# Kernel optimization log

Hardware: AMD Instinct MI355X
Metric: run time of the kernel (lower is better)

## Reference

```python
import jax, jax.numpy as jnp
import numpy as np

D_IN = 768
D_SAE = 24576
BATCH = 2048
K = 64


def setup_inputs() -> dict:
    key = jax.random.key(0)
    k1, k2 = jax.random.split(key)
    x = jax.random.normal(k1, (BATCH, D_IN), dtype=jnp.float32)
    # kaiming-uniform-ish init then unit-norm rows (set_decoder_norm_to_unit_norm)
    bound = np.sqrt(6.0 / D_SAE)
    W_dec = jax.random.uniform(k2, (D_SAE, D_IN), minval=-bound, maxval=bound, dtype=jnp.float32)
    W_dec = W_dec / jnp.linalg.norm(W_dec, axis=1, keepdims=True)
    W_enc = W_dec.T  # tied at init (W_dec.t().clone())
    b_enc = jnp.zeros((D_SAE,), dtype=jnp.float32)
    b_dec = jnp.zeros((D_IN,), dtype=jnp.float32)
    return {"x": x, "W_enc": W_enc, "W_dec": W_dec, "b_enc": b_enc, "b_dec": b_dec, "k": K}


def topk_activation(pre, k):
    # torch.topk -> relu(values) -> scatter into zeros
    vals, idx = jax.lax.top_k(pre, k)            # [B, k]
    vals = jax.nn.relu(vals)
    rows = jnp.arange(pre.shape[0])[:, None]     # [B, 1]
    return jnp.zeros_like(pre).at[rows, idx].set(vals)


def reference(x, W_enc, W_dec, b_enc, b_dec, k):
    # normalize=False -> preprocess is identity
    xc = x - b_dec
    latents_pre_act = xc @ W_enc + b_enc         # [B, d_sae]
    latents = topk_activation(latents_pre_act, k)
    recons = latents @ W_dec + b_dec             # [B, d_in]
    mse_loss = jnp.sum((recons - x) ** 2)        # F.mse_loss(reduction='sum')
    return mse_loss
```

## Files before the change

kernel.cpp:

```cpp
#include <hip/hip_runtime.h>
#include <hip/hip_bf16.h>
#include <stdint.h>
#include <string.h>

#define D_IN 768
#define D_SAE 24576
#define BATCH 2048
#define TOPK 64
#define CAP 1024
#define CAPB 120
#define KEY_LIM 0xC000u

typedef _Float16 f16x8 __attribute__((ext_vector_type(8)));
typedef _Float16 f16x4 __attribute__((ext_vector_type(4)));
typedef float floatx4 __attribute__((ext_vector_type(4)));

#define AS1 __attribute__((address_space(1)))
#define AS3 __attribute__((address_space(3)))

__device__ __forceinline__ void load_lds16(const void* g, void* l) {
    __builtin_amdgcn_global_load_lds((AS1 void*)(g), (AS3 void*)(l), 16, 0, 0);
}

__global__ __launch_bounds__(256) void prep_x_kernel(const float* __restrict__ x,
                                                     const float* __restrict__ b_dec,
                                                     _Float16* __restrict__ xch,
                                                     int* __restrict__ cnt,
                                                     float* __restrict__ out) {
    int t = blockIdx.x * 256 + threadIdx.x;
    if (t == 0) out[0] = 0.0f;
    if (t < BATCH) cnt[t] = 0;
    int i = t * 4;
    if (i >= BATCH * D_IN) return;
    int c = i % D_IN;
    float4 xv = *(const float4*)(x + i);
    float4 bv = *(const float4*)(b_dec + c);
    f16x4 h;
    h[0] = (_Float16)(xv.x - bv.x);
    h[1] = (_Float16)(xv.y - bv.y);
    h[2] = (_Float16)(xv.z - bv.z);
    h[3] = (_Float16)(xv.w - bv.w);
    *(f16x4*)(xch + i) = h;
}

__global__ __launch_bounds__(256) void transpose_kernel(const float* __restrict__ W,
                                                        _Float16* __restrict__ WT) {
    __shared__ _Float16 tile[32][33];
    int n0 = blockIdx.x * 32;
    int k0 = blockIdx.y * 32;
    int tx = threadIdx.x & 31, ty = threadIdx.x >> 5;
#pragma unroll
    for (int r = 0; r < 4; ++r) {
        int k = k0 + ty + r * 8;
        tile[ty + r * 8][tx] = (_Float16)W[(size_t)k * D_SAE + n0 + tx];
    }
    __syncthreads();
#pragma unroll
    for (int r = 0; r < 4; ++r) {
        int n = n0 + ty + r * 8;
        WT[(size_t)n * D_IN + k0 + tx] = tile[tx][ty + r * 8];
    }
}


#define TE 16384

#define BAR() do { __builtin_amdgcn_sched_barrier(0);            \
                   asm volatile("s_barrier" ::: "memory");       \
                   __builtin_amdgcn_sched_barrier(0); } while (0)
#define WLG() do { asm volatile("s_waitcnt lgkmcnt(0)" ::: "memory"); \
                   __builtin_amdgcn_sched_barrier(0); } while (0)

__global__ __launch_bounds__(512, 2) void gemm_kernel(const _Float16* __restrict__ A,
                                                      const _Float16* __restrict__ BT,
                                                      const float* __restrict__ b_enc,
                                                      int* __restrict__ cnt,
                                                      unsigned* __restrict__ cand) {
    __shared__ __align__(16) char smem[131072];
    _Float16* As = (_Float16*)smem;
    _Float16* Bs = (_Float16*)(smem + 65536);

    const int tid = threadIdx.x;
    const int lane = tid & 63;
    const int wave = tid >> 6;
    const int wm = wave >> 2;
    const int wn = wave & 3;

    const int bid = blockIdx.x;
    const int swz = (bid & 7) * 96 + (bid >> 3);
    const int m0 = (swz & 7) * 256;
    const int n0 = (swz >> 3) * 256;

    const int drow = lane >> 3;
    const int g8 = ((lane & 7) ^ drow) * 8;
    const _Float16* Ath = A + (size_t)(m0 + drow) * D_IN + g8;
    const _Float16* Bth = BT + (size_t)(n0 + drow) * D_IN + g8;
    const int arb = wave * 8;
    const int brb = ((wave >> 2) << 6) + (wave & 3) * 8;

    const int colv = lane & 15, quad = lane >> 4;
    const int sw = colv & 7;
    const int o0 = ((quad) ^ sw) * 8;
    const int o1 = ((quad + 4) ^ sw) * 8;
    const int amr = (wm * 128 + colv) * 64;
    const int bnr = (wn * 64 + colv) * 64;

    floatx4 acc[8][4];
#pragma unroll
    for (int mi = 0; mi < 8; ++mi)
#pragma unroll
        for (int ni = 0; ni < 4; ++ni)
#pragma unroll
            for (int r = 0; r < 4; ++r) acc[mi][ni][r] = 0.0f;

#define STA(CB, RB, KC) load_lds16(Ath + (size_t)(RB) * D_IN + (KC), As + (CB) * TE + (RB) * 64)
#define STB(CB, RB, KC) load_lds16(Bth + (size_t)(RB) * D_IN + (KC), Bs + (CB) * TE + (RB) * 64)

    STA(0, arb, 0);        STA(0, arb + 128, 0);
    STB(0, brb, 0);        STB(0, brb + 128, 0);
    STA(0, arb + 64, 0);   STA(0, arb + 192, 0);
    STB(0, brb + 32, 0);   STB(0, brb + 160, 0);
    STA(1, arb, 64);       STA(1, arb + 128, 64);
    STB(1, brb, 64);       STB(1, brb + 128, 64);
    STA(1, arb + 64, 64);  STA(1, arb + 192, 64);
    asm volatile("s_waitcnt vmcnt(6)" ::: "memory");
    BAR();

#define KTILE(KT, CB, S1, S2, VMN) do {                                            \
    const _Float16* Ac = As + (CB) * TE;                                           \
    const _Float16* Bc = Bs + (CB) * TE;                                           \
    const int kc1 = ((KT) + 1) * 64, kc2 = ((KT) + 2) * 64;                        \
    f16x8 alo[4][2], ahi[4][2], blo[2][2], bhi[2][2];                              \
                  \
    _Pragma("unroll") for (int mi = 0; mi < 4; ++mi) {                             \
        alo[mi][0] = *(const f16x8*)(Ac + amr + mi * 1024 + o0);                   \
        alo[mi][1] = *(const f16x8*)(Ac + amr + mi * 1024 + o1);                   \
    }                                                                              \
    _Pragma("unroll") for (int ni = 0; ni < 2; ++ni) {                             \
        blo[ni][0] = *(const f16x8*)(Bc + bnr + ni * 1024 + o0);                   \
        blo[ni][1] = *(const f16x8*)(Bc + bnr + ni * 1024 + o1);                   \
    }                                                                              \
    if (S1) { STB(1 - (CB), brb + 32, kc1); STB(1 - (CB), brb + 160, kc1); }       \
    BAR(); WLG();                                                                  \
    __builtin_amdgcn_s_setprio(1);                                                 \
    _Pragma("unroll") for (int mi = 0; mi < 4; ++mi)                               \
        _Pragma("unroll") for (int ni = 0; ni < 2; ++ni) {                         \
            acc[mi][ni] = __builtin_amdgcn_mfma_f32_16x16x32_f16(alo[mi][0], blo[ni][0], acc[mi][ni], 0, 0, 0); \
            acc[mi][ni] = __builtin_amdgcn_mfma_f32_16x16x32_f16(alo[mi][1], blo[ni][1], acc[mi][ni], 0, 0, 0); \
        }                                                                          \
    __builtin_amdgcn_s_setprio(0);                                                 \
    BAR();                                                                         \
             \
    _Pragma("unroll") for (int mi = 0; mi < 4; ++mi) {                             \
        ahi[mi][0] = *(const f16x8*)(Ac + amr + (mi + 4) * 1024 + o0);             \
        ahi[mi][1] = *(const f16x8*)(Ac + amr + (mi + 4) * 1024 + o1);             \
    }                                                                              \
    if (S2) { STA(CB, arb, kc2); STA(CB, arb + 128, kc2); }                        \
    BAR(); WLG();                                                                  \
    __builtin_amdgcn_s_setprio(1);                                                 \
    _Pragma("unroll") for (int mi = 0; mi < 4; ++mi)                               \
        _Pragma("unroll") for (int ni = 0; ni < 2; ++ni) {                         \
            acc[mi + 4][ni] = __builtin_amdgcn_mfma_f32_16x16x32_f16(ahi[mi][0], blo[ni][0], acc[mi + 4][ni], 0, 0, 0); \
            acc[mi + 4][ni] = __builtin_amdgcn_mfma_f32_16x16x32_f16(ahi[mi][1], blo[ni][1], acc[mi + 4][ni], 0, 0, 0); \
        }                                                                          \
    __builtin_amdgcn_s_setprio(0);                                                 \
    BAR();                                                                         \
             \
    _Pragma("unroll") for (int ni = 0; ni < 2; ++ni) {                             \
        bhi[ni][0] = *(const f16x8*)(Bc + bnr + (ni + 2) * 1024 + o0);             \
        bhi[ni][1] = *(const f16x8*)(Bc + bnr + (ni + 2) * 1024 + o1);             \
    }                                                                              \
    if (S2) { STB(CB, brb, kc2); STB(CB, brb + 128, kc2); }                        \
    BAR(); WLG();                                                                  \
    __builtin_amdgcn_s_setprio(1);                                                 \
    _Pragma("unroll") for (int mi = 0; mi < 4; ++mi)                               \
        _Pragma("unroll") for (int ni = 0; ni < 2; ++ni) {                         \
            acc[mi + 4][ni + 2] = __builtin_amdgcn_mfma_f32_16x16x32_f16(ahi[mi][0], bhi[ni][0], acc[mi + 4][ni + 2], 0, 0, 0); \
            acc[mi + 4][ni + 2] = __builtin_amdgcn_mfma_f32_16x16x32_f16(ahi[mi][1], bhi[ni][1], acc[mi + 4][ni + 2], 0, 0, 0); \
        }                                                                          \
    __builtin_amdgcn_s_setprio(0);                                                 \
    BAR();                                                                         \
         \
    if (S2) { STA(CB, arb + 64, kc2); STA(CB, arb + 192, kc2); }                   \
    BAR(); WLG();                                                                  \
    __builtin_amdgcn_s_setprio(1);                                                 \
    _Pragma("unroll") for (int mi = 0; mi < 4; ++mi)                               \
        _Pragma("unroll") for (int ni = 0; ni < 2; ++ni) {                         \
            acc[mi][ni + 2] = __builtin_amdgcn_mfma_f32_16x16x32_f16(alo[mi][0], bhi[ni][0], acc[mi][ni + 2], 0, 0, 0); \
            acc[mi][ni + 2] = __builtin_amdgcn_mfma_f32_16x16x32_f16(alo[mi][1], bhi[ni][1], acc[mi][ni + 2], 0, 0, 0); \
        }                                                                          \
    __builtin_amdgcn_s_setprio(0);                                                 \
    if (VMN == 6) asm volatile("s_waitcnt vmcnt(6)" ::: "memory");                 \
    else if (VMN == 0) asm volatile("s_waitcnt vmcnt(0)" ::: "memory");            \
    BAR();                                                                         \
} while (0)

    for (int kp = 0; kp < 5; ++kp) {
        const int kte = kp * 2;
        KTILE(kte, 0, 1, 1, 6);
        KTILE(kte + 1, 1, 1, 1, 6);
    }
    KTILE(10, 0, 1, 0, 0);
    KTILE(11, 1, 0, 0, -1);

#undef KTILE
#undef STA
#undef STB

    __syncthreads();
    int* lcnt      = (int*)smem;
    int* gbase     = (int*)(smem + 1024);
    unsigned* lbuf = (unsigned*)(smem + 2048);

    if (tid < 256) lcnt[tid] = 0;
    __syncthreads();

    float be[4];
#pragma unroll
    for (int ni = 0; ni < 4; ++ni) be[ni] = b_enc[n0 + wn * 64 + ni * 16 + colv];
#pragma unroll
    for (int mi = 0; mi < 8; ++mi) {
#pragma unroll
        for (int ni = 0; ni < 4; ++ni) {
            const int n_g = n0 + wn * 64 + ni * 16 + colv;
            const int lrow0 = wm * 128 + mi * 16 + quad * 4;
#pragma unroll
            for (int r = 0; r < 4; ++r) {
                _Float16 h = (_Float16)(acc[mi][ni][r] + be[ni]);
                unsigned short u;
                __builtin_memcpy(&u, &h, 2);
                unsigned key = (unsigned)(u ^ ((u & 0x8000) ? 0xFFFFu : 0x8000u));
                if (key >= KEY_LIM) {
                    int lrow = lrow0 + r;
                    int ls = atomicAdd(&lcnt[lrow], 1);
                    if (ls < CAPB) lbuf[lrow * CAPB + ls] = (key << 16) | (unsigned)n_g;
                }
            }
        }
    }
    __syncthreads();

    if (tid < 256) {
        int c = lcnt[tid];
        int g = 0;
        if (c > 0) {
            int add = (c <= CAPB) ? c : (c + CAP + 1);
            g = atomicAdd(&cnt[m0 + tid], add);
        }
        gbase[tid] = g;
    }
    __syncthreads();

    if (tid < 256) {
        int c = lcnt[tid]; if (c > CAPB) c = CAPB;
        int g = gbase[tid];
        unsigned* dst = cand + (size_t)(m0 + tid) * CAP;
        for (int j = 0; j < c; ++j) {
            int p = g + j;
            if (p < CAP) dst[p] = lbuf[tid * CAPB + j];
        }
    }
}

__global__ __launch_bounds__(256) void topk_loss_kernel(const unsigned* __restrict__ cand,
                                                        const int* __restrict__ cnt,
                                                        const _Float16* __restrict__ xch,
                                                        const _Float16* __restrict__ WT,
                                                        const float* __restrict__ b_enc,
                                                        const float* __restrict__ x,
                                                        const float* __restrict__ b_dec,
                                                        unsigned short* __restrict__ scratch,
                                                        float* __restrict__ out) {
    const int row = blockIdx.x;
    const int tid = threadIdx.x;
    const int lane = tid & 63, wv = tid >> 6;

    __shared__ unsigned cl[CAP];
    __shared__ int hist[256];
    __shared__ int wtot[4];
    __shared__ float wred[4];
    __shared__ int sh_B, sh_K, na, ne;
    __shared__ int sel_idx[TOPK];
    __shared__ float sel_val[TOPK];
    __shared__ _Float16 xs[D_IN];

    const int n_raw = cnt[row];
    const bool fast = (n_raw >= TOPK && n_raw <= CAP);
    const int N = fast ? n_raw : D_SAE;
    unsigned short* prow = scratch + (size_t)row * D_SAE;

    if (fast) {
        const unsigned* cr = cand + (size_t)row * CAP;
        for (int i = tid; i < N; i += 256) cl[i] = cr[i];
    } else {
        const _Float16* xr = xch + (size_t)row * D_IN;
        for (int i = tid; i < D_IN; i += 256) xs[i] = xr[i];
        __syncthreads();
        for (int j = tid; j < D_SAE; j += 256) {
            float s = b_enc[j];
            const _Float16* wr = WT + (size_t)j * D_IN;
            for (int k = 0; k < D_IN; ++k) s += (float)xs[k] * (float)wr[k];
            _Float16 h = (_Float16)s;
            unsigned short u;
            __builtin_memcpy(&u, &h, 2);
            prow[j] = (unsigned short)(u ^ ((u & 0x8000) ? 0xFFFFu : 0x8000u));
        }
    }
    __syncthreads();

    int K = TOPK;

    hist[tid] = 0;
    __syncthreads();
    for (int i = tid; i < N; i += 256) {
        unsigned k = fast ? (cl[i] >> 24) : ((unsigned)prow[i] >> 8);
        atomicAdd(&hist[k], 1);
    }
    __syncthreads();
    {
        int h = hist[tid], s = h;
#pragma unroll
        for (int off = 1; off < 64; off <<= 1) {
            int v = __shfl_down(s, off, 64);
            if (lane + off < 64) s += v;
        }
        if (lane == 0) wtot[wv] = s;
        __syncthreads();
        for (int w2 = wv + 1; w2 < 4; ++w2) s += wtot[w2];
        int G = s - h;
        if (G < K && s >= K) { sh_B = tid; sh_K = K - G; }
        __syncthreads();
    }
    const unsigned B = (unsigned)sh_B;
    K = sh_K;
    __syncthreads();

    hist[tid] = 0;
    __syncthreads();
    for (int i = tid; i < N; i += 256) {
        unsigned k = fast ? (cl[i] >> 16) : (unsigned)prow[i];
        if ((k >> 8) == B) atomicAdd(&hist[k & 0xFF], 1);
    }
    __syncthreads();
    {
        int h = hist[tid], s = h;
#pragma unroll
        for (int off = 1; off < 64; off <<= 1) {
            int v = __shfl_down(s, off, 64);
            if (lane + off < 64) s += v;
        }
        if (lane == 0) wtot[wv] = s;
        __syncthreads();
        for (int w2 = wv + 1; w2 < 4; ++w2) s += wtot[w2];
        int G = s - h;
        if (G < K && s >= K) { sh_B = tid; sh_K = K - G; }
        __syncthreads();
    }
    const unsigned T = (B << 8) | (unsigned)sh_B;
    const int K2 = sh_K;
    const int nGreater = TOPK - K2;

    if (tid == 0) { na = 0; ne = 0; }
    __syncthreads();
    for (int i = tid; i < N; i += 256) {
        unsigned k; int col;
        if (fast) { unsigned v = cl[i]; k = v >> 16; col = (int)(v & 0xFFFFu); }
        else      { k = (unsigned)prow[i]; col = i; }
        int slot = -1;
        if (k > T) slot = atomicAdd(&na, 1);
        else if (k == T) {
            int e = atomicAdd(&ne, 1);
            if (e < K2) slot = nGreater + e;
        }
        if (slot >= 0) {
            unsigned short u = (unsigned short)((k & 0x8000u) ? (k ^ 0x8000u) : (k ^ 0xFFFFu));
            _Float16 h;
            __builtin_memcpy(&h, &u, 2);
            sel_idx[slot] = col;
            sel_val[slot] = fmaxf((float)h, 0.0f);
        }
    }
    __syncthreads();

    const int c0 = tid, c1 = tid + 256, c2 = tid + 512;
    const float* xr = x + (size_t)row * D_IN;
    float r0 = b_dec[c0], r1 = b_dec[c1], r2 = b_dec[c2];
#pragma unroll 8
    for (int s = 0; s < TOPK; ++s) {
        float v = sel_val[s];
        const _Float16* wr = WT + (size_t)sel_idx[s] * D_IN;
        r0 += v * (float)wr[c0];
        r1 += v * (float)wr[c1];
        r2 += v * (float)wr[c2];
    }
    float d0 = r0 - xr[c0], d1 = r1 - xr[c1], d2 = r2 - xr[c2];
    float local = d0 * d0 + d1 * d1 + d2 * d2;

#pragma unroll
    for (int off = 32; off > 0; off >>= 1) local += __shfl_down(local, off, 64);
    if (lane == 0) wred[wv] = local;
    __syncthreads();
    if (tid == 0) atomicAdd(out, wred[0] + wred[1] + wred[2] + wred[3]);
}

extern "C" void kernel_launch(void* const* d_in, const int* in_sizes, int n_in,
                              void* d_out, int out_size, void* d_ws, size_t ws_size,
                              hipStream_t stream) {
    const float* x     = (const float*)d_in[0];
    const float* W_enc = (const float*)d_in[1];
    const float* W_dec = (const float*)d_in[2];
    const float* b_enc = (const float*)d_in[3];
    const float* b_dec = (const float*)d_in[4];
    float* out = (float*)d_out;

    char* ws = (char*)d_ws;
    _Float16* xch           = (_Float16*)ws;
    _Float16* WT            = (_Float16*)(ws + 3145728);
    unsigned short* scratch = (unsigned short*)(ws + 3145728 + 37748736);
    int* cnt                = (int*)(ws + 3145728 + 37748736 + 100663296);
    unsigned* cand          = (unsigned*)(ws + 3145728 + 37748736 + 100663296 + 8192);

    prep_x_kernel<<<1536, 256, 0, stream>>>(x, b_dec, xch, cnt, out);
    transpose_kernel<<<dim3(D_SAE / 32, D_IN / 32), 256, 0, stream>>>(W_enc, WT);
    gemm_kernel<<<dim3(768), 512, 0, stream>>>(xch, WT, b_enc, cnt, cand);
    topk_loss_kernel<<<BATCH, 256, 0, stream>>>(cand, cnt, xch, WT, b_enc, x, b_dec, scratch, out);
}
```

Before: 319.2 us.

## Replace global atomic candidate append with fixed per-block slots

The GEMM epilogue no longer does a global atomicAdd per row to append candidates. Each block now writes its count plus up to 30 candidates into a fixed slot indexed by (row, column block), which removes the global counter and its zeroing. The top-k kernel sums the 96 slot counts with an LDS prefix and gathers the candidates into shared memory. The fallback path now recomputes keys on the fly instead of staging them in a scratch buffer, so it does three full dot-product passes and becomes much slower. The lower per-block cap also makes that fallback more likely to trigger.

```diff
diff --git a/kernel.cpp b/kernel.cpp
--- a/kernel.cpp
+++ b/kernel.cpp
@@ -8,7 +8,9 @@
 #define BATCH 2048
 #define TOPK 64
 #define CAP 1024
-#define CAPB 120
+#define NBLK 96
+#define SLOTW 32
+#define CAPB_L 30
 #define KEY_LIM 0xC000u
 
 typedef _Float16 f16x8 __attribute__((ext_vector_type(8)));
@@ -25,11 +27,9 @@
 __global__ __launch_bounds__(256) void prep_x_kernel(const float* __restrict__ x,
                                                      const float* __restrict__ b_dec,
                                                      _Float16* __restrict__ xch,
-                                                     int* __restrict__ cnt,
                                                      float* __restrict__ out) {
     int t = blockIdx.x * 256 + threadIdx.x;
     if (t == 0) out[0] = 0.0f;
-    if (t < BATCH) cnt[t] = 0;
     int i = t * 4;
     if (i >= BATCH * D_IN) return;
     int c = i % D_IN;
@@ -74,7 +74,6 @@
 __global__ __launch_bounds__(512, 2) void gemm_kernel(const _Float16* __restrict__ A,
                                                       const _Float16* __restrict__ BT,
                                                       const float* __restrict__ b_enc,
-                                                      int* __restrict__ cnt,
                                                       unsigned* __restrict__ cand) {
     __shared__ __align__(16) char smem[131072];
     _Float16* As = (_Float16*)smem;
@@ -209,8 +208,7 @@
 
     __syncthreads();
     int* lcnt      = (int*)smem;
-    int* gbase     = (int*)(smem + 1024);
-    unsigned* lbuf = (unsigned*)(smem + 2048);
+    unsigned* lbuf = (unsigned*)(smem + 1024);
 
     if (tid < 256) lcnt[tid] = 0;
     __syncthreads();
@@ -233,7 +231,7 @@
                 if (key >= KEY_LIM) {
                     int lrow = lrow0 + r;
                     int ls = atomicAdd(&lcnt[lrow], 1);
-                    if (ls < CAPB) lbuf[lrow * CAPB + ls] = (key << 16) | (unsigned)n_g;
+                    if (ls < CAPB_L) lbuf[lrow * CAPB_L + ls] = (key << 16) | (unsigned)n_g;
                 }
             }
         }
@@ -242,34 +240,19 @@
 
     if (tid < 256) {
         int c = lcnt[tid];
-        int g = 0;
-        if (c > 0) {
-            int add = (c <= CAPB) ? c : (c + CAP + 1);
-            g = atomicAdd(&cnt[m0 + tid], add);
-        }
-        gbase[tid] = g;
-    }
-    __syncthreads();
-
-    if (tid < 256) {
-        int c = lcnt[tid]; if (c > CAPB) c = CAPB;
-        int g = gbase[tid];
-        unsigned* dst = cand + (size_t)(m0 + tid) * CAP;
-        for (int j = 0; j < c; ++j) {
-            int p = g + j;
-            if (p < CAP) dst[p] = lbuf[tid * CAPB + j];
-        }
+        unsigned* slot = cand + ((size_t)(m0 + tid) * NBLK + (n0 >> 8)) * SLOTW;
+        slot[0] = (unsigned)c;
+        int cc = c > CAPB_L ? CAPB_L : c;
+        for (int j = 0; j < cc; ++j) slot[1 + j] = lbuf[tid * CAPB_L + j];
     }
 }
 
 __global__ __launch_bounds__(256) void topk_loss_kernel(const unsigned* __restrict__ cand,
-                                                        const int* __restrict__ cnt,
                                                         const _Float16* __restrict__ xch,
                                                         const _Float16* __restrict__ WT,
                                                         const float* __restrict__ b_enc,
                                                         const float* __restrict__ x,
                                                         const float* __restrict__ b_dec,
-                                                        unsigned short* __restrict__ scratch,
                                                         float* __restrict__ out) {
     const int row = blockIdx.x;
     const int tid = threadIdx.x;
@@ -280,40 +263,51 @@
     __shared__ int wtot[4];
     __shared__ float wred[4];
     __shared__ int sh_B, sh_K, na, ne;
+    __shared__ int s_tot, s_over;
     __shared__ int sel_idx[TOPK];
     __shared__ float sel_val[TOPK];
     __shared__ _Float16 xs[D_IN];
 
-    const int n_raw = cnt[row];
-    const bool fast = (n_raw >= TOPK && n_raw <= CAP);
+    const unsigned* rs = cand + (size_t)row * NBLK * SLOTW;
+    if (tid == 0) { s_tot = 0; s_over = 0; }
+    __syncthreads();
+    int myb = 0, myc = 0;
+    if (tid < NBLK) {
+        int c = (int)rs[(size_t)tid * SLOTW];
+        if (c > CAPB_L) { s_over = 1; c = 0; }
+        myc = c;
+        if (c) myb = atomicAdd(&s_tot, c);
+    }
+    __syncthreads();
+    const int n_raw = s_tot;
+    const bool fast = (!s_over && n_raw >= TOPK && n_raw <= CAP);
     const int N = fast ? n_raw : D_SAE;
-    unsigned short* prow = scratch + (size_t)row * D_SAE;
 
     if (fast) {
-        const unsigned* cr = cand + (size_t)row * CAP;
-        for (int i = tid; i < N; i += 256) cl[i] = cr[i];
+        if (tid < NBLK)
+            for (int j = 0; j < myc; ++j) cl[myb + j] = rs[(size_t)tid * SLOTW + 1 + j];
     } else {
         const _Float16* xr = xch + (size_t)row * D_IN;
         for (int i = tid; i < D_IN; i += 256) xs[i] = xr[i];
-        __syncthreads();
-        for (int j = tid; j < D_SAE; j += 256) {
-            float s = b_enc[j];
-            const _Float16* wr = WT + (size_t)j * D_IN;
-            for (int k = 0; k < D_IN; ++k) s += (float)xs[k] * (float)wr[k];
-            _Float16 h = (_Float16)s;
-            unsigned short u;
-            __builtin_memcpy(&u, &h, 2);
-            prow[j] = (unsigned short)(u ^ ((u & 0x8000) ? 0xFFFFu : 0x8000u));
-        }
-    }
-    __syncthreads();
+    }
+    __syncthreads();
+
+    auto keyof = [&](int j) -> unsigned {
+        float s = b_enc[j];
+        const _Float16* wr = WT + (size_t)j * D_IN;
+        for (int k = 0; k < D_IN; ++k) s += (float)xs[k] * (float)wr[k];
+        _Float16 h = (_Float16)s;
+        unsigned short u;
+        __builtin_memcpy(&u, &h, 2);
+        return (unsigned)(u ^ ((u & 0x8000) ? 0xFFFFu : 0x8000u));
+    };
 
     int K = TOPK;
 
     hist[tid] = 0;
     __syncthreads();
     for (int i = tid; i < N; i += 256) {
-        unsigned k = fast ? (cl[i] >> 24) : ((unsigned)prow[i] >> 8);
+        unsigned k = fast ? (cl[i] >> 24) : (keyof(i) >> 8);
         atomicAdd(&hist[k], 1);
     }
     __syncthreads();
@@ -338,7 +332,7 @@
     hist[tid] = 0;
     __syncthreads();
     for (int i = tid; i < N; i += 256) {
-        unsigned k = fast ? (cl[i] >> 16) : (unsigned)prow[i];
+        unsigned k = fast ? (cl[i] >> 16) : keyof(i);
         if ((k >> 8) == B) atomicAdd(&hist[k & 0xFF], 1);
     }
     __syncthreads();
@@ -365,7 +359,7 @@
     for (int i = tid; i < N; i += 256) {
         unsigned k; int col;
         if (fast) { unsigned v = cl[i]; k = v >> 16; col = (int)(v & 0xFFFFu); }
-        else      { k = (unsigned)prow[i]; col = i; }
+        else      { k = keyof(i); col = i; }
         int slot = -1;
         if (k > T) slot = atomicAdd(&na, 1);
         else if (k == T) {
@@ -414,14 +408,12 @@
     float* out = (float*)d_out;
 
     char* ws = (char*)d_ws;
-    _Float16* xch           = (_Float16*)ws;
-    _Float16* WT            = (_Float16*)(ws + 3145728);
-    unsigned short* scratch = (unsigned short*)(ws + 3145728 + 37748736);
-    int* cnt                = (int*)(ws + 3145728 + 37748736 + 100663296);
-    unsigned* cand          = (unsigned*)(ws + 3145728 + 37748736 + 100663296 + 8192);
-
-    prep_x_kernel<<<1536, 256, 0, stream>>>(x, b_dec, xch, cnt, out);
+    _Float16* xch = (_Float16*)ws;
+    _Float16* WT  = (_Float16*)(ws + 3145728);
+    unsigned* cand = (unsigned*)(ws + 3145728 + 37748736);
+
+    prep_x_kernel<<<1536, 256, 0, stream>>>(x, b_dec, xch, out);
     transpose_kernel<<<dim3(D_SAE / 32, D_IN / 32), 256, 0, stream>>>(W_enc, WT);
-    gemm_kernel<<<dim3(768), 512, 0, stream>>>(xch, WT, b_enc, cnt, cand);
-    topk_loss_kernel<<<BATCH, 256, 0, stream>>>(cand, cnt, xch, WT, b_enc, x, b_dec, scratch, out);
-}
+    gemm_kernel<<<dim3(768), 512, 0, stream>>>(xch, WT, b_enc, cand);
+    topk_loss_kernel<<<BATCH, 256, 0, stream>>>(cand, xch, WT, b_enc, x, b_dec, out);
+}
```

Result: no change. 323.4 us (+1.3%).
